# Optimization experiments

Hardware: AMD Instinct MI355X
Metric: run time of the kernel (lower is better)

## Reference

```python
import jax, jax.numpy as jnp
import numpy as np

B, S, D, H = 16, 8192, 512, 512
NEG_INF = -1e18


def setup_inputs() -> dict:
    key0 = jax.random.key(0)
    ks = jax.random.split(key0, 8)
    scale = 1.0 / np.sqrt(D)
    return {
        "query": jax.random.normal(ks[0], (B, D), dtype=jnp.float32),
        "key": jax.random.normal(ks[1], (B, S, D), dtype=jnp.float32),
        "mask": jax.random.bernoulli(ks[2], 0.1, (B, S)),
        # q_proj: Linear(D -> H) with bias
        "Wq": jax.random.uniform(ks[3], (H, D), jnp.float32, -scale, scale),
        "bq": jax.random.uniform(ks[4], (H,), jnp.float32, -scale, scale),
        # k_proj: Conv1d(D -> H, kernel=1) == pointwise Linear with bias
        "Wk": jax.random.uniform(ks[5], (H, D), jnp.float32, -scale, scale),
        "bk": jax.random.uniform(ks[6], (H,), jnp.float32, -scale, scale),
        # out_proj: Linear(H -> 1, bias=False), init uniform(-1, 1)
        "w_out": jax.random.uniform(ks[7], (H,), jnp.float32, -1.0, 1.0),
    }


def reference(query, key, mask, Wq, bq, Wk, bk, w_out):
    # q_proj: (B, D) -> (B, H)
    q_h = query @ Wq.T + bq
    # k_proj (1x1 conv): (B, S, D) -> (B, S, H)
    k_h = jnp.einsum("bsd,hd->bsh", key, Wk) + bk
    # score = w_out . (q_h broadcast + k_h)  -> (B, S)
    attn_weight = jnp.einsum("bsh,h->bs", q_h[:, None, :] + k_h, w_out)
    attn_weight = jnp.where(mask, NEG_INF, attn_weight)
    attn_prob = jax.nn.softmax(attn_weight, axis=-1)
    # weighted sum over projected keys: (B, H)
    attn = jnp.einsum("bsh,bs->bh", k_h, attn_prob)
    return attn, attn_weight
```

## Files before the change

### kernel.cpp

```cpp
#include <hip/hip_runtime.h>
#include <math.h>

#define BB 16
#define SS 8192
#define DD 512
#define HH 512
#define NEG_INF (-1e18f)
#define BPB 64

__device__ __forceinline__ float dot8(float4 a0, float4 a1, float4 b0, float4 b1) {
  return a0.x*b0.x + a0.y*b0.y + a0.z*b0.z + a0.w*b0.w
       + a1.x*b1.x + a1.y*b1.y + a1.z*b1.z + a1.w*b1.w;
}

__device__ __forceinline__ float wave_sum64(float p) {
  #pragma unroll
  for (int off = 32; off; off >>= 1) p += __shfl_xor(p, off, 64);
  return p;
}

__global__ __launch_bounds__(256) void k_gemv(
    const float* __restrict__ Wq, const float* __restrict__ Wk,
    const float* __restrict__ wout, float* __restrict__ wpart,
    float* __restrict__ vpart)
{
  int blk = blockIdx.x;
  int tid = threadIdx.x;
  int j = blk & 15;
  const float* W = (blk < 16) ? Wk : Wq;
  float* outp = (blk < 16) ? vpart : wpart;
  float a0 = 0.f, a1 = 0.f;
  #pragma unroll 8
  for (int h = j * 32; h < j * 32 + 32; ++h) {
    float w = wout[h];
    a0 += w * W[(size_t)h * DD + tid];
    a1 += w * W[(size_t)h * DD + tid + 256];
  }
  outp[j * DD + tid] = a0;
  outp[j * DD + tid + 256] = a1;
}

__global__ __launch_bounds__(512) void k_fin(
    const float* __restrict__ query, const float* __restrict__ vpart,
    const float* __restrict__ wpart, const float* __restrict__ wout,
    const float* __restrict__ bq, const float* __restrict__ bk,
    float* __restrict__ v, float* __restrict__ qconst)
{
  int tid = threadIdx.x;
  float a = 0.f, w = 0.f;
  #pragma unroll
  for (int j = 0; j < 16; ++j) {
    a += vpart[j * DD + tid];
    w += wpart[j * DD + tid];
  }
  v[tid] = a;

  __shared__ __align__(16) float w2s[DD];
  __shared__ float red[8];
  __shared__ float c0s;
  w2s[tid] = w;
  float cpart = wave_sum64(wout[tid] * (bq[tid] + bk[tid]));
  int wv = tid >> 6, ln = tid & 63;
  if (ln == 0) red[wv] = cpart;
  __syncthreads();
  if (tid == 0) {
    float c = 0.f;
    #pragma unroll
    for (int i = 0; i < 8; ++i) c += red[i];
    c0s = c;
  }
  __syncthreads();

  const float4* w24 = (const float4*)w2s;
  float4 x0 = w24[ln], x1 = w24[64 + ln];
  float c0 = c0s;
  #pragma unroll
  for (int t = 0; t < 2; ++t) {
    int b = wv * 2 + t;
    const float4* q4 = (const float4*)(query + (size_t)b * DD);
    float p = wave_sum64(dot8(q4[ln], q4[64 + ln], x0, x1));
    if (ln == 0) qconst[b] = p + c0;
  }
}

__global__ __launch_bounds__(256) void k_score(
    const float* __restrict__ key, const int* __restrict__ mask,
    const float* __restrict__ v, const float* __restrict__ qconst,
    float* __restrict__ scores, float* __restrict__ partials)
{
  int blk = blockIdx.x;
  int b = blk / BPB;
  int pb = blk % BPB;
  const int rows = SS / BPB;
  int s0 = pb * rows;
  int wave = threadIdx.x >> 6;
  int lane = threadIdx.x & 63;

  const float4* vv = (const float4*)v;
  float4 v0 = vv[lane], v1 = vv[64 + lane];
  float qc = qconst[b];
  const float4* keyb = (const float4*)(key + (size_t)b * SS * DD);
  const int* maskb = mask + b * SS;

  float m = -INFINITY, l = 0.f;
  float4 u0 = {0.f,0.f,0.f,0.f}, u1 = {0.f,0.f,0.f,0.f};

  const int nit = rows / 16;
  int s = s0 + wave * 4;

  float4 r0a, r0b, r1a, r1b, r2a, r2b, r3a, r3b;
  {
    const float4* p0 = keyb + (size_t)s * (DD / 4);
    r0a = p0[lane];       r0b = p0[64 + lane];
    r1a = p0[128 + lane]; r1b = p0[192 + lane];
    r2a = p0[256 + lane]; r2b = p0[320 + lane];
    r3a = p0[384 + lane]; r3b = p0[448 + lane];
  }
  int4 mk = *(const int4*)(maskb + s);

  for (int i = 0; i < nit; ++i) {
    float4 n0a=r0a, n0b=r0b, n1a=r1a, n1b=r1b, n2a=r2a, n2b=r2b, n3a=r3a, n3b=r3b;
    int4 nmk = {0,0,0,0};
    if (i + 1 < nit) {
      const float4* p0 = keyb + (size_t)(s + 16) * (DD / 4);
      n0a = p0[lane];       n0b = p0[64 + lane];
      n1a = p0[128 + lane]; n1b = p0[192 + lane];
      n2a = p0[256 + lane]; n2b = p0[320 + lane];
      n3a = p0[384 + lane]; n3b = p0[448 + lane];
      nmk = *(const int4*)(maskb + s + 16);
    }
    float p0v = dot8(r0a, r0b, v0, v1);
    float p1v = dot8(r1a, r1b, v0, v1);
    float p2v = dot8(r2a, r2b, v0, v1);
    float p3v = dot8(r3a, r3b, v0, v1);
    #pragma unroll
    for (int off = 32; off; off >>= 1) {
      p0v += __shfl_xor(p0v, off, 64);
      p1v += __shfl_xor(p1v, off, 64);
      p2v += __shfl_xor(p2v, off, 64);
      p3v += __shfl_xor(p3v, off, 64);
    }
    float sc0 = mk.x ? NEG_INF : (p0v + qc);
    float sc1 = mk.y ? NEG_INF : (p1v + qc);
    float sc2 = mk.z ? NEG_INF : (p2v + qc);
    float sc3 = mk.w ? NEG_INF : (p3v + qc);
    if (lane == 0) {
      float4 st = {sc0, sc1, sc2, sc3};
      *(float4*)(scores + (size_t)b * SS + s) = st;
    }
    float mn = fmaxf(fmaxf(fmaxf(sc0, sc1), fmaxf(sc2, sc3)), m);
    if (mn > m) {
      float sc = __expf(m - mn);
      l *= sc;
      u0.x *= sc; u0.y *= sc; u0.z *= sc; u0.w *= sc;
      u1.x *= sc; u1.y *= sc; u1.z *= sc; u1.w *= sc;
      m = mn;
    }
    float e0 = __expf(sc0 - m), e1 = __expf(sc1 - m);
    float e2 = __expf(sc2 - m), e3 = __expf(sc3 - m);
    l += (e0 + e1) + (e2 + e3);
    u0.x += e0*r0a.x + e1*r1a.x + e2*r2a.x + e3*r3a.x;
    u0.y += e0*r0a.y + e1*r1a.y + e2*r2a.y + e3*r3a.y;
    u0.z += e0*r0a.z + e1*r1a.z + e2*r2a.z + e3*r3a.z;
    u0.w += e0*r0a.w + e1*r1a.w + e2*r2a.w + e3*r3a.w;
    u1.x += e0*r0b.x + e1*r1b.x + e2*r2b.x + e3*r3b.x;
    u1.y += e0*r0b.y + e1*r1b.y + e2*r2b.y + e3*r3b.y;
    u1.z += e0*r0b.z + e1*r1b.z + e2*r2b.z + e3*r3b.z;
    u1.w += e0*r0b.w + e1*r1b.w + e2*r2b.w + e3*r3b.w;
    r0a=n0a; r0b=n0b; r1a=n1a; r1b=n1b; r2a=n2a; r2b=n2b; r3a=n3a; r3b=n3b;
    mk = nmk; s += 16;
  }

  __shared__ float ls_m[4], ls_l[4];
  __shared__ __align__(16) float ls_u[4][DD];
  ls_u[wave][4 * lane + 0] = u0.x; ls_u[wave][4 * lane + 1] = u0.y;
  ls_u[wave][4 * lane + 2] = u0.z; ls_u[wave][4 * lane + 3] = u0.w;
  ls_u[wave][256 + 4 * lane + 0] = u1.x; ls_u[wave][256 + 4 * lane + 1] = u1.y;
  ls_u[wave][256 + 4 * lane + 2] = u1.z; ls_u[wave][256 + 4 * lane + 3] = u1.w;
  if (lane == 0) { ls_m[wave] = m; ls_l[wave] = l; }
  __syncthreads();

  float M = fmaxf(fmaxf(ls_m[0], ls_m[1]), fmaxf(ls_m[2], ls_m[3]));
  float f0 = __expf(ls_m[0] - M), f1 = __expf(ls_m[1] - M);
  float f2 = __expf(ls_m[2] - M), f3 = __expf(ls_m[3] - M);
  int d = threadIdx.x;
  float ua = ls_u[0][d] * f0 + ls_u[1][d] * f1 + ls_u[2][d] * f2 + ls_u[3][d] * f3;
  float ub = ls_u[0][d + 256] * f0 + ls_u[1][d + 256] * f1
           + ls_u[2][d + 256] * f2 + ls_u[3][d + 256] * f3;
  float* part = partials + (size_t)(b * BPB + pb) * (DD + 2);
  part[2 + d] = ua;
  part[2 + 256 + d] = ub;
  if (threadIdx.x == 0) {
    part[0] = M;
    part[1] = ls_l[0] * f0 + ls_l[1] * f1 + ls_l[2] * f2 + ls_l[3] * f3;
  }
}

__global__ __launch_bounds__(256) void k_comb(
    const float* __restrict__ partials, float* __restrict__ ubar)
{
  int b = blockIdx.x;
  int tid = threadIdx.x;
  __shared__ float fsh[BPB];
  __shared__ float dsh;
  const float* pbase = partials + (size_t)b * BPB * (DD + 2);

  if (tid < 64) {
    float mp = pbase[tid * (DD + 2)];
    float lp = pbase[tid * (DD + 2) + 1];
    float M = mp;
    #pragma unroll
    for (int off = 32; off; off >>= 1) M = fmaxf(M, __shfl_xor(M, off, 64));
    float f = __expf(mp - M);
    fsh[tid] = f;
    float dn = wave_sum64(lp * f);
    if (tid == 0) dsh = dn;
  }
  __syncthreads();

  float inv = 1.f / dsh;
  float ua = 0.f, ub_ = 0.f;
  #pragma unroll 8
  for (int p = 0; p < BPB; ++p) {
    float f = fsh[p];
    ua  += pbase[p * (DD + 2) + 2 + tid] * f;
    ub_ += pbase[p * (DD + 2) + 2 + 256 + tid] * f;
  }
  ubar[b * DD + tid] = ua * inv;
  ubar[b * DD + tid + 256] = ub_ * inv;
}

__global__ __launch_bounds__(256) void k_attn(
    const float* __restrict__ Wk, const float* __restrict__ bk,
    const float* __restrict__ ubar, float* __restrict__ attn)
{
  int b = blockIdx.x >> 4;
  int hc = blockIdx.x & 15;
  int wave = threadIdx.x >> 6, lane = threadIdx.x & 63;
  const float4* ub4 = (const float4*)(ubar + (size_t)b * DD);
  float4 x0 = ub4[lane], x1 = ub4[64 + lane];
  #pragma unroll
  for (int j = 0; j < 8; ++j) {
    int h = hc * 32 + wave * 8 + j;
    const float4* wr = (const float4*)(Wk + (size_t)h * DD);
    float p = wave_sum64(dot8(wr[lane], wr[64 + lane], x0, x1));
    if (lane == 0) attn[b * HH + h] = p + bk[h];
  }
}

extern "C" void kernel_launch(void* const* d_in, const int* in_sizes, int n_in,
                              void* d_out, int out_size, void* d_ws, size_t ws_size,
                              hipStream_t stream) {
  const float* query = (const float*)d_in[0];
  const float* key   = (const float*)d_in[1];
  const int*   mask  = (const int*)d_in[2];
  const float* Wq    = (const float*)d_in[3];
  const float* bq    = (const float*)d_in[4];
  const float* Wk    = (const float*)d_in[5];
  const float* bk    = (const float*)d_in[6];
  const float* wout  = (const float*)d_in[7];

  float* out    = (float*)d_out;
  float* attn   = out;
  float* scores = out + BB * HH;
  float* ws     = (float*)d_ws;

  const size_t off_v    = 0;
  const size_t off_qc   = 512;
  const size_t off_ubar = 528;
  const size_t off_scr  = off_ubar + BB * DD;
  float* vpart    = ws + off_scr;
  float* wpart    = ws + off_scr + 16 * DD;
  float* partials = ws + off_scr;

  k_gemv<<<dim3(32), dim3(256), 0, stream>>>(Wq, Wk, wout, wpart, vpart);
  k_fin<<<dim3(1), dim3(512), 0, stream>>>(query, vpart, wpart, wout, bq, bk,
                                           ws + off_v, ws + off_qc);
  k_score<<<dim3(BB * BPB), dim3(256), 0, stream>>>(key, mask, ws + off_v, ws + off_qc,
                                                    scores, partials);
  k_comb<<<dim3(BB), dim3(256), 0, stream>>>(partials, ws + off_ubar);
  k_attn<<<dim3(BB * 16), dim3(256), 0, stream>>>(Wk, bk, ws + off_ubar, attn);
}
```

Before: 69.09 us.

## Fuse prep and tail kernels, use DPP wave reductions

Pipeline drops from five kernels to three. The two GEMV/finalize kernels merge into one 129-block prep kernel with a shared-memory tree reduction, and the per-batch query constant is now computed inside the score kernel. The combine and output-projection kernels are fused, so each of the 256 blocks recomputes the normalized ubar redundantly. Shuffle-based wave reductions are replaced with DPP row/broadcast reductions read from lane 63, and the score kernel gets a launch-bounds occupancy hint. The aim is to cut launch overhead and reduction latency, at the cost of redundant partial-combine reads in k_out.

```diff
diff --git a/kernel.cpp b/kernel.cpp
--- a/kernel.cpp
+++ b/kernel.cpp
@@ -13,79 +13,89 @@
        + a1.x*b1.x + a1.y*b1.y + a1.z*b1.z + a1.w*b1.w;
 }
 
-__device__ __forceinline__ float wave_sum64(float p) {
-  #pragma unroll
-  for (int off = 32; off; off >>= 1) p += __shfl_xor(p, off, 64);
-  return p;
-}
-
-__global__ __launch_bounds__(256) void k_gemv(
+template <int CTRL>
+__device__ __forceinline__ float dpp_add0(float x) {
+  return x + __int_as_float(__builtin_amdgcn_update_dpp(
+      0, __float_as_int(x), CTRL, 0xf, 0xf, true));
+}
+__device__ __forceinline__ float wave_red_sum(float x) {
+  x = dpp_add0<0x111>(x);
+  x = dpp_add0<0x112>(x);
+  x = dpp_add0<0x114>(x);
+  x = dpp_add0<0x118>(x);
+  x = dpp_add0<0x142>(x);
+  x = dpp_add0<0x143>(x);
+  return x;
+}
+__device__ __forceinline__ float lane63(float x) {
+  return __int_as_float(__builtin_amdgcn_readlane(__float_as_int(x), 63));
+}
+template <int CTRL>
+__device__ __forceinline__ float dpp_maxstep(float x) {
+  int y = __builtin_amdgcn_update_dpp(
+      __float_as_int(x), __float_as_int(x), CTRL, 0xf, 0xf, false);
+  return fmaxf(x, __int_as_float(y));
+}
+__device__ __forceinline__ float wave_red_max(float x) {
+  x = dpp_maxstep<0x111>(x); x = dpp_maxstep<0x112>(x);
+  x = dpp_maxstep<0x114>(x); x = dpp_maxstep<0x118>(x);
+  x = dpp_maxstep<0x142>(x); x = dpp_maxstep<0x143>(x);
+  return x;
+}
+
+__global__ __launch_bounds__(256) void k_prep(
     const float* __restrict__ Wq, const float* __restrict__ Wk,
-    const float* __restrict__ wout, float* __restrict__ wpart,
-    float* __restrict__ vpart)
+    const float* __restrict__ wout, const float* __restrict__ bq,
+    const float* __restrict__ bk, float* __restrict__ v,
+    float* __restrict__ w2, float* __restrict__ c0)
 {
   int blk = blockIdx.x;
-  int tid = threadIdx.x;
-  int j = blk & 15;
-  const float* W = (blk < 16) ? Wk : Wq;
-  float* outp = (blk < 16) ? vpart : wpart;
-  float a0 = 0.f, a1 = 0.f;
-  #pragma unroll 8
-  for (int h = j * 32; h < j * 32 + 32; ++h) {
-    float w = wout[h];
-    a0 += w * W[(size_t)h * DD + tid];
-    a1 += w * W[(size_t)h * DD + tid + 256];
-  }
-  outp[j * DD + tid] = a0;
-  outp[j * DD + tid + 256] = a1;
-}
-
-__global__ __launch_bounds__(512) void k_fin(
-    const float* __restrict__ query, const float* __restrict__ vpart,
-    const float* __restrict__ wpart, const float* __restrict__ wout,
-    const float* __restrict__ bq, const float* __restrict__ bk,
-    float* __restrict__ v, float* __restrict__ qconst)
-{
-  int tid = threadIdx.x;
-  float a = 0.f, w = 0.f;
+  int t = threadIdx.x;
+  if (blk == 128) {
+    if (t < 64) {
+      float part = 0.f;
+      #pragma unroll
+      for (int i = 0; i < 8; ++i) {
+        int h = t + 64 * i;
+        part += wout[h] * (bq[h] + bk[h]);
+      }
+      part = wave_red_sum(part);
+      if (t == 63) c0[0] = part;
+    }
+    return;
+  }
+  int j = blk & 63;
+  const float* W = (blk < 64) ? Wk : Wq;
+  float* outp = (blk < 64) ? v : w2;
+  int dsl = j * 8;
+  int h0 = t, h1 = t + 256;
+  const float4* r0 = (const float4*)(W + (size_t)h0 * DD + dsl);
+  const float4* r1 = (const float4*)(W + (size_t)h1 * DD + dsl);
+  float4 a0 = r0[0], a1 = r0[1], b0 = r1[0], b1 = r1[1];
+  float wA = wout[h0], wB = wout[h1];
+  float acc[8];
+  acc[0] = wA*a0.x + wB*b0.x; acc[1] = wA*a0.y + wB*b0.y;
+  acc[2] = wA*a0.z + wB*b0.z; acc[3] = wA*a0.w + wB*b0.w;
+  acc[4] = wA*a1.x + wB*b1.x; acc[5] = wA*a1.y + wB*b1.y;
+  acc[6] = wA*a1.z + wB*b1.z; acc[7] = wA*a1.w + wB*b1.w;
+  __shared__ float red[256][9];
   #pragma unroll
-  for (int j = 0; j < 16; ++j) {
-    a += vpart[j * DD + tid];
-    w += wpart[j * DD + tid];
-  }
-  v[tid] = a;
-
-  __shared__ __align__(16) float w2s[DD];
-  __shared__ float red[8];
-  __shared__ float c0s;
-  w2s[tid] = w;
-  float cpart = wave_sum64(wout[tid] * (bq[tid] + bk[tid]));
-  int wv = tid >> 6, ln = tid & 63;
-  if (ln == 0) red[wv] = cpart;
-  __syncthreads();
-  if (tid == 0) {
-    float c = 0.f;
-    #pragma unroll
-    for (int i = 0; i < 8; ++i) c += red[i];
-    c0s = c;
-  }
-  __syncthreads();
-
-  const float4* w24 = (const float4*)w2s;
-  float4 x0 = w24[ln], x1 = w24[64 + ln];
-  float c0 = c0s;
-  #pragma unroll
-  for (int t = 0; t < 2; ++t) {
-    int b = wv * 2 + t;
-    const float4* q4 = (const float4*)(query + (size_t)b * DD);
-    float p = wave_sum64(dot8(q4[ln], q4[64 + ln], x0, x1));
-    if (ln == 0) qconst[b] = p + c0;
-  }
-}
-
-__global__ __launch_bounds__(256) void k_score(
+  for (int k = 0; k < 8; ++k) red[t][k] = acc[k];
+  __syncthreads();
+  for (int st = 128; st; st >>= 1) {
+    if (t < st) {
+      #pragma unroll
+      for (int k = 0; k < 8; ++k) red[t][k] += red[t + st][k];
+    }
+    __syncthreads();
+  }
+  if (t < 8) outp[dsl + t] = red[0][t];
+}
+
+__global__ __launch_bounds__(256, 4) void k_score(
     const float* __restrict__ key, const int* __restrict__ mask,
-    const float* __restrict__ v, const float* __restrict__ qconst,
+    const float* __restrict__ query, const float* __restrict__ ws_v,
+    const float* __restrict__ ws_w2, const float* __restrict__ ws_c0,
     float* __restrict__ scores, float* __restrict__ partials)
 {
   int blk = blockIdx.x;
@@ -96,9 +106,17 @@
   int wave = threadIdx.x >> 6;
   int lane = threadIdx.x & 63;
 
-  const float4* vv = (const float4*)v;
+  const float4* vv = (const float4*)ws_v;
   float4 v0 = vv[lane], v1 = vv[64 + lane];
-  float qc = qconst[b];
+
+  float qc;
+  {
+    const float4* q4 = (const float4*)(query + (size_t)b * DD);
+    const float4* w24 = (const float4*)ws_w2;
+    float qp = wave_red_sum(dot8(q4[lane], q4[64 + lane], w24[lane], w24[64 + lane]));
+    qc = lane63(qp) + ws_c0[0];
+  }
+
   const float4* keyb = (const float4*)(key + (size_t)b * SS * DD);
   const int* maskb = mask + b * SS;
 
@@ -129,21 +147,16 @@
       n3a = p0[384 + lane]; n3b = p0[448 + lane];
       nmk = *(const int4*)(maskb + s + 16);
     }
-    float p0v = dot8(r0a, r0b, v0, v1);
-    float p1v = dot8(r1a, r1b, v0, v1);
-    float p2v = dot8(r2a, r2b, v0, v1);
-    float p3v = dot8(r3a, r3b, v0, v1);
-    #pragma unroll
-    for (int off = 32; off; off >>= 1) {
-      p0v += __shfl_xor(p0v, off, 64);
-      p1v += __shfl_xor(p1v, off, 64);
-      p2v += __shfl_xor(p2v, off, 64);
-      p3v += __shfl_xor(p3v, off, 64);
-    }
-    float sc0 = mk.x ? NEG_INF : (p0v + qc);
-    float sc1 = mk.y ? NEG_INF : (p1v + qc);
-    float sc2 = mk.z ? NEG_INF : (p2v + qc);
-    float sc3 = mk.w ? NEG_INF : (p3v + qc);
+    float p0v = wave_red_sum(dot8(r0a, r0b, v0, v1));
+    float p1v = wave_red_sum(dot8(r1a, r1b, v0, v1));
+    float p2v = wave_red_sum(dot8(r2a, r2b, v0, v1));
+    float p3v = wave_red_sum(dot8(r3a, r3b, v0, v1));
+    float d0 = lane63(p0v), d1 = lane63(p1v);
+    float d2 = lane63(p2v), d3 = lane63(p3v);
+    float sc0 = mk.x ? NEG_INF : (d0 + qc);
+    float sc1 = mk.y ? NEG_INF : (d1 + qc);
+    float sc2 = mk.z ? NEG_INF : (d2 + qc);
+    float sc3 = mk.w ? NEG_INF : (d3 + qc);
     if (lane == 0) {
       float4 st = {sc0, sc1, sc2, sc3};
       *(float4*)(scores + (size_t)b * SS + s) = st;
@@ -196,11 +209,15 @@
   }
 }
 
-__global__ __launch_bounds__(256) void k_comb(
-    const float* __restrict__ partials, float* __restrict__ ubar)
+__global__ __launch_bounds__(256) void k_out(
+    const float* __restrict__ Wk, const float* __restrict__ bk,
+    const float* __restrict__ partials, float* __restrict__ attn)
 {
-  int b = blockIdx.x;
+  int b = blockIdx.x >> 4;
+  int hc = blockIdx.x & 15;
   int tid = threadIdx.x;
+  int wave = tid >> 6, lane = tid & 63;
+  __shared__ __align__(16) float ubar[DD];
   __shared__ float fsh[BPB];
   __shared__ float dsh;
   const float* pbase = partials + (size_t)b * BPB * (DD + 2);
@@ -208,13 +225,11 @@
   if (tid < 64) {
     float mp = pbase[tid * (DD + 2)];
     float lp = pbase[tid * (DD + 2) + 1];
-    float M = mp;
-    #pragma unroll
-    for (int off = 32; off; off >>= 1) M = fmaxf(M, __shfl_xor(M, off, 64));
+    float M = lane63(wave_red_max(mp));
     float f = __expf(mp - M);
     fsh[tid] = f;
-    float dn = wave_sum64(lp * f);
-    if (tid == 0) dsh = dn;
+    float dn = wave_red_sum(lp * f);
+    if (tid == 63) dsh = dn;
   }
   __syncthreads();
 
@@ -226,25 +241,18 @@
     ua  += pbase[p * (DD + 2) + 2 + tid] * f;
     ub_ += pbase[p * (DD + 2) + 2 + 256 + tid] * f;
   }
-  ubar[b * DD + tid] = ua * inv;
-  ubar[b * DD + tid + 256] = ub_ * inv;
-}
-
-__global__ __launch_bounds__(256) void k_attn(
-    const float* __restrict__ Wk, const float* __restrict__ bk,
-    const float* __restrict__ ubar, float* __restrict__ attn)
-{
-  int b = blockIdx.x >> 4;
-  int hc = blockIdx.x & 15;
-  int wave = threadIdx.x >> 6, lane = threadIdx.x & 63;
-  const float4* ub4 = (const float4*)(ubar + (size_t)b * DD);
+  ubar[tid] = ua * inv;
+  ubar[tid + 256] = ub_ * inv;
+  __syncthreads();
+
+  const float4* ub4 = (const float4*)ubar;
   float4 x0 = ub4[lane], x1 = ub4[64 + lane];
   #pragma unroll
   for (int j = 0; j < 8; ++j) {
     int h = hc * 32 + wave * 8 + j;
     const float4* wr = (const float4*)(Wk + (size_t)h * DD);
-    float p = wave_sum64(dot8(wr[lane], wr[64 + lane], x0, x1));
-    if (lane == 0) attn[b * HH + h] = p + bk[h];
+    float p = wave_red_sum(dot8(wr[lane], wr[64 + lane], x0, x1));
+    if (lane == 63) attn[b * HH + h] = p + bk[h];
   }
 }
 
@@ -265,19 +273,14 @@
   float* scores = out + BB * HH;
   float* ws     = (float*)d_ws;
 
-  const size_t off_v    = 0;
-  const size_t off_qc   = 512;
-  const size_t off_ubar = 528;
-  const size_t off_scr  = off_ubar + BB * DD;
-  float* vpart    = ws + off_scr;
-  float* wpart    = ws + off_scr + 16 * DD;
-  float* partials = ws + off_scr;
-
-  k_gemv<<<dim3(32), dim3(256), 0, stream>>>(Wq, Wk, wout, wpart, vpart);
-  k_fin<<<dim3(1), dim3(512), 0, stream>>>(query, vpart, wpart, wout, bq, bk,
-                                           ws + off_v, ws + off_qc);
-  k_score<<<dim3(BB * BPB), dim3(256), 0, stream>>>(key, mask, ws + off_v, ws + off_qc,
-                                                    scores, partials);
-  k_comb<<<dim3(BB), dim3(256), 0, stream>>>(partials, ws + off_ubar);
-  k_attn<<<dim3(BB * 16), dim3(256), 0, stream>>>(Wk, bk, ws + off_ubar, attn);
-}
+  float* ws_v  = ws;
+  float* ws_w2 = ws + 512;
+  float* ws_c0 = ws + 1024;
+  float* partials = ws + 1040;
+
+  k_prep<<<dim3(129), dim3(256), 0, stream>>>(Wq, Wk, wout, bq, bk,
+                                              ws_v, ws_w2, ws_c0);
+  k_score<<<dim3(BB * BPB), dim3(256), 0, stream>>>(key, mask, query, ws_v,
+                                                    ws_w2, ws_c0, scores, partials);
+  k_out<<<dim3(BB * 16), dim3(256), 0, stream>>>(Wk, bk, partials, attn);
+}
```

After: 60.97 us (median of 2 runs). -11.8%, faster.
